# Kernel optimization log

Hardware: AMD Instinct MI355X
Metric: run time of the kernel (lower is better)

## Reference

```python
import jax, jax.numpy as jnp
import numpy as np

N_ATOMS = 50_000
N_EDGES = 1_600_000
N_ANGLES = 1_500_000
N_SPECIES = 16
DIM = 64
HID = [64, 64, 64]
IN_DIM = 1 + 2 * N_SPECIES  # theta + two onehot species encodings


def setup_inputs() -> dict:
    key = jax.random.key(0)
    ks = jax.random.split(key, 16)
    species = jax.random.randint(ks[0], (N_ATOMS,), 0, N_SPECIES)
    edge_dst = jax.random.randint(ks[1], (N_EDGES,), 0, N_ATOMS)
    # distances strictly positive (avoid blowup in 1/d)
    distances = jax.random.uniform(ks[2], (N_EDGES,), jnp.float32, 0.5, 1.5)
    switch = jax.random.uniform(ks[3], (N_EDGES,), jnp.float32)
    vec = jax.random.normal(ks[4], (N_EDGES, 3), jnp.float32)
    angle_src = jax.random.randint(ks[5], (N_ANGLES,), 0, N_EDGES)
    angle_dst = jax.random.randint(ks[6], (N_ANGLES,), 0, N_EDGES)
    central_atom = jax.random.randint(ks[7], (N_ANGLES,), 0, N_ATOMS)
    # FullyConnectedNet([64,64,64,64]) params, shared across the two calls
    dims = [IN_DIM] + HID + [DIM]
    params = {}
    for i in range(len(dims) - 1):
        fan_in = dims[i]
        params[f"W{i}"] = jax.random.normal(ks[8 + i], (dims[i], dims[i + 1]), jnp.float32) / np.sqrt(fan_in)
        params[f"b{i}"] = jnp.zeros((dims[i + 1],), jnp.float32)
    return dict(species=species, edge_dst=edge_dst, distances=distances,
                switch=switch, vec=vec, angle_src=angle_src, angle_dst=angle_dst,
                central_atom=central_atom, **params)


def _mlp(x, W0, b0, W1, b1, W2, b2, W3, b3):
    h = jax.nn.silu(x @ W0 + b0)
    h = jax.nn.silu(h @ W1 + b1)
    h = jax.nn.silu(h @ W2 + b2)
    return h @ W3 + b3  # linear output layer


def reference(species, edge_dst, distances, switch, vec, angle_src, angle_dst,
              central_atom, W0, b0, W1, b1, W2, b2, W3, b3):
    onehot = jax.nn.one_hot(species, N_SPECIES, dtype=jnp.float32)  # [N, 16]
    d = distances[:, None]
    sw = switch[:, None]
    vecn = vec / d
    sij = sw / d  # divide_distances=True
    Rij = jnp.concatenate((sij, sij * vecn), axis=-1)  # [E, 4]
    zdest = onehot[edge_dst]  # [E, 16]
    z_angsrc = zdest[angle_src]  # [A, 16]
    z_angdst = zdest[angle_dst]  # [A, 16]
    theta = jnp.sum(Rij[angle_src] * Rij[angle_dst], axis=-1, keepdims=True)  # [A, 1]
    Gijk = (_mlp(jnp.concatenate((theta, z_angsrc, z_angdst), axis=-1), W0, b0, W1, b1, W2, b2, W3, b3)
            + _mlp(jnp.concatenate((theta, z_angdst, z_angsrc), axis=-1), W0, b0, W1, b1, W2, b2, W3, b3))
    embedding = jax.ops.segment_sum(Gijk * theta, central_atom, species.shape[0])  # [N, 64]
    return embedding
```

## Files before the change

kernel.cpp:

```cpp
#include <hip/hip_runtime.h>

#define N_ATOMS   50000
#define N_EDGES   1600000
#define N_ANGLES  1500000
#define SCAN_B    196

#define NT      256
#define UMAX    4.852092f
#define H_U     0.038055623f
#define INV_HU  26.277306f
#define TSZ     (136 * NT * 64)

#define E_BLK   6250
#define P_BLK   112
#define Z_BLK   196

#define B_BLK   272
#define A_BLK   5860
#define R_BLK   8704
#define M_BLK   5860

typedef unsigned short u16;
typedef unsigned int   u32;
typedef _Float16 f16x8 __attribute__((ext_vector_type(8)));
typedef float    f32x4 __attribute__((ext_vector_type(4)));
typedef u16      u16x8 __attribute__((ext_vector_type(8)));

__device__ __forceinline__ float silu_f(float x) {
    return __fdividef(x, 1.0f + __expf(-x));
}
__device__ __forceinline__ u16 f2h(float x) {
    _Float16 h = (_Float16)x;
    return __builtin_bit_cast(u16, h);
}
__device__ __forceinline__ float h2f(u16 u) {
    return (float)__builtin_bit_cast(_Float16, u);
}

__global__ __launch_bounds__(256) void fused_prep_kernel(
    const float* __restrict__ distances, const float* __restrict__ sw,
    const float* __restrict__ vec, const int* __restrict__ edge_dst,
    const int* __restrict__ species,
    const float* __restrict__ W0, const float* __restrict__ b0,
    const float* __restrict__ W1, const float* __restrict__ W2,
    const float* __restrict__ W3,
    float2* __restrict__ EC8,
    u16* __restrict__ WT1, u16* __restrict__ WT2, u16* __restrict__ WT3,
    float* __restrict__ base_tab, int* __restrict__ cnt)
{
    const int bid = (int)blockIdx.x;
    const int tid = (int)threadIdx.x;

    if (bid < E_BLK) {
        int e = bid * 256 + tid;
        if (e >= N_EDGES) return;
        const float d   = distances[e];
        const float s   = sw[e];
        const float inv = 1.0f / d;
        const float sij = s * inv;
        const float c   = sij * inv;
        const int   sp  = species[edge_dst[e]];
        u16 h0 = f2h(sij);
        u16 h1 = f2h(c * vec[3*e+0]);
        u16 h2 = f2h(c * vec[3*e+1]);
        u16 h3 = f2h(c * vec[3*e+2]);
        h0 = (h0 & 0xFFFEu) | ((u16)( sp       & 1));
        h1 = (h1 & 0xFFFEu) | ((u16)((sp >> 1) & 1));
        h2 = (h2 & 0xFFFEu) | ((u16)((sp >> 2) & 1));
        h3 = (h3 & 0xFFFEu) | ((u16)((sp >> 3) & 1));
        const u32 lo = (u32)h0 | ((u32)h1 << 16);
        const u32 hi = (u32)h2 | ((u32)h3 << 16);
        EC8[e] = make_float2(__uint_as_float(lo), __uint_as_float(hi));
    } else if (bid < E_BLK + P_BLK) {
        int t = (bid - E_BLK) * 256 + tid;
        if (t < 3 * 4096) {
            int l = t >> 12, e = t & 4095, n = e >> 6, k = e & 63;
            const float* W = (l == 0) ? W1 : (l == 1) ? W2 : W3;
            u16* WT        = (l == 0) ? WT1 : (l == 1) ? WT2 : WT3;
            WT[n*64 + k] = f2h(W[k*64 + n]);
        }
        int u = t - 3 * 4096;
        if (u >= 0 && u < 256 * 64) {
            int sd = u >> 6, j = u & 63, s = sd >> 4, d = sd & 15;
            base_tab[u] = W0[(1+s)*64 + j] + W0[(17+d)*64 + j] + b0[j];
        }
    } else {
        int idx = (bid - E_BLK - P_BLK) * 256 + tid;
        if (idx < N_ATOMS) cnt[idx] = 0;
    }
}

__device__ __forceinline__ u32 make_rec(float2 Es, float2 Ed) {
    const u32 slo = __float_as_uint(Es.x), shi = __float_as_uint(Es.y);
    const u32 dlo = __float_as_uint(Ed.x), dhi = __float_as_uint(Ed.y);
    const int s1 = (int)((slo & 1u) | ((slo >> 15) & 2u)
                       | ((shi & 1u) << 2) | ((shi >> 13) & 8u));
    const int s2 = (int)((dlo & 1u) | ((dlo >> 15) & 2u)
                       | ((dhi & 1u) << 2) | ((dhi >> 13) & 8u));
    const float theta = h2f((u16)slo) * h2f((u16)dlo)
                      + h2f((u16)(slo >> 16)) * h2f((u16)(dlo >> 16))
                      + h2f((u16)shi) * h2f((u16)dhi)
                      + h2f((u16)(shi >> 16)) * h2f((u16)(dhi >> 16));
    const int s = min(s1, s2), d = max(s1, s2);
    const int pid = s*16 - (s*(s-1))/2 + (d - s);

    const float x  = theta * 0.125f;
    const float ax = fabsf(x);
    float uu = __logf(ax + __fsqrt_rn(fmaf(ax, ax, 1.0f)));
    uu = copysignf(uu, x);
    const float tt = fminf(fmaxf(fmaf(uu, INV_HU, UMAX * INV_HU), 0.0f),
                           (float)NT - 1.001f);
    const u32 tfx = (u32)(tt * 32768.0f);
    return (tfx << 8) | (u32)pid;
}

__device__ __forceinline__ void dense_mfma(const u16* __restrict__ strip,
    const u16* __restrict__ WT, int r15, int g4, f32x4 acc[4][4])
{
    #pragma unroll
    for (int kt = 0; kt < 2; ++kt) {
        f16x8 A[4], B[4];
        #pragma unroll
        for (int mt = 0; mt < 4; ++mt) {
            int row = mt*16 + r15;
            int col = (kt*32 + g4*8) ^ ((row & 7) << 3);
            A[mt] = *(const f16x8*)&strip[row*64 + col];
        }
        #pragma unroll
        for (int nt = 0; nt < 4; ++nt)
            B[nt] = *(const f16x8*)&WT[(nt*16 + r15)*64 + kt*32 + g4*8];
        #pragma unroll
        for (int mt = 0; mt < 4; ++mt) {
            #pragma unroll
            for (int nt = 0; nt < 4; ++nt)
                acc[mt][nt] = __builtin_amdgcn_mfma_f32_16x16x32_f16(
                    A[mt], B[nt], acc[mt][nt], 0, 0, 0);
        }
    }
}

__device__ __forceinline__ void act_store(u16* __restrict__ strip,
    const float* __restrict__ bias, int r15, int g4, f32x4 acc[4][4])
{
    float bn[4];
    #pragma unroll
    for (int nt = 0; nt < 4; ++nt) bn[nt] = bias[nt*16 + r15];
    #pragma unroll
    for (int mt = 0; mt < 4; ++mt) {
        #pragma unroll
        for (int r = 0; r < 4; ++r) {
            int row = mt*16 + g4*4 + r;
            int rsw = (row & 7) << 3;
            #pragma unroll
            for (int nt = 0; nt < 4; ++nt)
                strip[row*64 + ((nt*16 + r15) ^ rsw)] =
                    f2h(silu_f(acc[mt][nt][r] + bn[nt]));
        }
    }
}

__global__ __launch_bounds__(256) void angle_build_kernel(
    const int* __restrict__ a_src, const int* __restrict__ a_dst,
    const int* __restrict__ a_ca, const float2* __restrict__ EC8,
    int* __restrict__ cnt, u32* __restrict__ car, u32* __restrict__ recU,
    const float* __restrict__ W0, const float* __restrict__ base_tab,
    const u16* __restrict__ WT1, const u16* __restrict__ WT2,
    const u16* __restrict__ WT3,
    const float* __restrict__ b1, const float* __restrict__ b2,
    const float* __restrict__ b3,
    u16* __restrict__ Tp)
{
    __shared__ __align__(16) u16 act[256 * 64];
    const int bid = (int)blockIdx.x;
    const int tid = (int)threadIdx.x;

    if (bid >= B_BLK) {
        int i = (bid - B_BLK) * 256 + tid;
        if (i >= N_ANGLES) return;
        const int se = a_src[i], de = a_dst[i], ca = a_ca[i];
        const float2 Es = EC8[se], Ed = EC8[de];
        const u32 rank = (u32)atomicAdd(&cnt[ca], 1);
        car[i]  = (rank << 18) | (u32)ca;
        recU[i] = make_rec(Es, Ed);
        return;
    }

    const int lane = tid & 63;
    const int wv   = tid >> 6;
    const int r15  = lane & 15;
    const int g4   = lane >> 4;

    const int pid = bid >> 1;
    const int m   = bid & 1;
    int s = 0, rem = pid;
    while (rem >= 16 - s) { rem -= 16 - s; ++s; }
    const int d = s + rem;

    const int idx = tid;
    const float u  = fmaf((float)idx, H_U, -UMAX);
    const float eu = __expf(u);
    const float theta = 4.0f * (eu - __frcp_rn(eu));

    u16* strip = act + wv * 4096;

    f32x4 accG[4][4];
    #pragma unroll
    for (int nt = 0; nt < 4; ++nt) {
        float bv = b3[nt*16 + r15];
        #pragma unroll
        for (int mt = 0; mt < 4; ++mt) accG[mt][nt] = {bv, bv, bv, bv};
    }

    {
        const int p = m ? (d*16 + s) : (s*16 + d);
        const float4* bs4 = (const float4*)(base_tab + p*64);
        const float4* w04 = (const float4*)W0;
        const int rsw = (lane & 7) << 3;
        #pragma unroll
        for (int c = 0; c < 8; ++c) {
            float4 bl = bs4[2*c], bh = bs4[2*c+1];
            float4 wl = w04[2*c], wh = w04[2*c+1];
            u16x8 hv;
            hv[0] = f2h(silu_f(fmaf(theta, wl.x, bl.x)));
            hv[1] = f2h(silu_f(fmaf(theta, wl.y, bl.y)));
            hv[2] = f2h(silu_f(fmaf(theta, wl.z, bl.z)));
            hv[3] = f2h(silu_f(fmaf(theta, wl.w, bl.w)));
            hv[4] = f2h(silu_f(fmaf(theta, wh.x, bh.x)));
            hv[5] = f2h(silu_f(fmaf(theta, wh.y, bh.y)));
            hv[6] = f2h(silu_f(fmaf(theta, wh.z, bh.z)));
            hv[7] = f2h(silu_f(fmaf(theta, wh.w, bh.w)));
            *(u16x8*)&strip[lane*64 + ((c*8) ^ rsw)] = hv;
        }
    }
    {
        f32x4 acc[4][4];
        #pragma unroll
        for (int mt = 0; mt < 4; ++mt)
            #pragma unroll
            for (int nt = 0; nt < 4; ++nt) acc[mt][nt] = {0.f,0.f,0.f,0.f};
        dense_mfma(strip, WT1, r15, g4, acc);
        act_store(strip, b1, r15, g4, acc);
    }
    {
        f32x4 acc[4][4];
        #pragma unroll
        for (int mt = 0; mt < 4; ++mt)
            #pragma unroll
            for (int nt = 0; nt < 4; ++nt) acc[mt][nt] = {0.f,0.f,0.f,0.f};
        dense_mfma(strip, WT2, r15, g4, acc);
        act_store(strip, b2, r15, g4, acc);
    }
    dense_mfma(strip, WT3, r15, g4, accG);

    #pragma unroll
    for (int mt = 0; mt < 4; ++mt) {
        #pragma unroll
        for (int r = 0; r < 4; ++r) {
            int row = mt*16 + g4*4 + r;
            int rsw = (row & 7) << 3;
            #pragma unroll
            for (int nt = 0; nt < 4; ++nt)
                strip[row*64 + ((nt*16 + r15) ^ rsw)] = f2h(accG[mt][nt][r]);
        }
    }
    __syncthreads();

    u16* dst = Tp + (size_t)m * TSZ + ((size_t)pid * NT + (size_t)idx) * 64;
    const int rsw = (tid & 7) << 3;
    #pragma unroll
    for (int c = 0; c < 8; ++c)
        *(u16x8*)(dst + c*8) = *(const u16x8*)&act[tid*64 + ((c*8) ^ rsw)];
}

__global__ __launch_bounds__(1024) void scanAB_kernel(
    const int* __restrict__ cnt, int* __restrict__ boff)
{
    __shared__ int sh[1024];
    const int t = (int)threadIdx.x;
    const int base = t * 64;
    int v = 0;
    #pragma unroll 8
    for (int k = 0; k < 64; ++k) {
        int idx = base + k;
        if (idx < N_ATOMS) v += cnt[idx];
    }
    sh[t] = v;
    __syncthreads();
    for (int off = 1; off < 1024; off <<= 1) {
        int u = (t >= off) ? sh[t - off] : 0;
        __syncthreads();
        sh[t] += u;
        __syncthreads();
    }
    if ((t & 3) == 0 && (t >> 2) < SCAN_B) boff[t >> 2] = sh[t] - v;
}

__global__ __launch_bounds__(256) void scanC_kernel(
    const int* __restrict__ cnt, const int* __restrict__ boff,
    int* __restrict__ cursor)
{
    __shared__ int sh[256];
    const int t = (int)threadIdx.x;
    const int idx = (int)blockIdx.x * 256 + t;
    int v = (idx < N_ATOMS) ? cnt[idx] : 0;
    sh[t] = v;
    __syncthreads();
    for (int off = 1; off < 256; off <<= 1) {
        int u = (t >= off) ? sh[t - off] : 0;
        __syncthreads();
        sh[t] += u;
        __syncthreads();
    }
    if (idx < N_ATOMS) {
        cursor[idx] = boff[blockIdx.x] + sh[t] - v;
        if (idx == N_ATOMS - 1) cursor[N_ATOMS] = boff[blockIdx.x] + sh[t];
    }
}

__global__ __launch_bounds__(256) void permute_repack_kernel(
    const u32* __restrict__ recU, const u32* __restrict__ car,
    const int* __restrict__ cursor, u32* __restrict__ rec,
    const u16* __restrict__ Tp, u32* __restrict__ T2)
{
    const int bid = (int)blockIdx.x;
    const int tid = (int)threadIdx.x;

    if (bid < R_BLK) {
        int idx = bid * 256 + tid;
        if (idx >= TSZ) return;
        const int row = (idx >> 6) & (NT - 1);
        const int nxt = (row < NT - 1) ? idx + 64 : idx;
        const int rown = (row < NT - 1) ? row + 1 : row;
        const float ua  = fmaf((float)row,  H_U, -UMAX);
        const float ub  = fmaf((float)rown, H_U, -UMAX);
        const float ea  = __expf(ua), eb = __expf(ub);
        const float tha = 4.0f * (ea - __frcp_rn(ea));
        const float thb = 4.0f * (eb - __frcp_rn(eb));
        const float ha = (h2f(Tp[idx]) + h2f(Tp[TSZ + idx])) * tha;
        const float hb = (h2f(Tp[nxt]) + h2f(Tp[TSZ + nxt])) * thb;
        T2[idx] = (u32)f2h(ha) | ((u32)f2h(hb) << 16);
    } else {
        int i = (bid - R_BLK) * 256 + tid;
        if (i >= N_ANGLES) return;
        const u32 cr = car[i];
        const int ca   = (int)(cr & 0x3FFFFu);
        const int rank = (int)(cr >> 18);
        rec[cursor[ca] + rank] = recU[i];
    }
}

__global__ __launch_bounds__(256) void lookup_kernel(
    const u32* __restrict__ rec, const int* __restrict__ cursor,
    const u32* __restrict__ T2, float* __restrict__ out)
{
    const int tid  = (int)threadIdx.x;
    const int lane = tid & 63;
    const int wv   = tid >> 6;
    const int atom = (int)blockIdx.x * 4 + wv;
    if (atom >= N_ATOMS) return;

    const int start = cursor[atom];
    const int end   = cursor[atom + 1];

    float acc0 = 0.f, acc1 = 0.f, acc2 = 0.f, acc3 = 0.f;
    for (int base = start; base < end; base += 64) {
        const int len = min(64, end - base);
        const int wp  = (int)rec[base + min(lane, len - 1)];

        int j = 0;
        for (; j + 3 < len; j += 4) {
            const u32 w0 = (u32)__shfl(wp, j),     w1 = (u32)__shfl(wp, j + 1);
            const u32 w2 = (u32)__shfl(wp, j + 2), w3 = (u32)__shfl(wp, j + 3);
            const u32 pr0 = T2[((w0 & 255u) << 14) + ((w0 >> 23) << 6) + (u32)lane];
            const u32 pr1 = T2[((w1 & 255u) << 14) + ((w1 >> 23) << 6) + (u32)lane];
            const u32 pr2 = T2[((w2 & 255u) << 14) + ((w2 >> 23) << 6) + (u32)lane];
            const u32 pr3 = T2[((w3 & 255u) << 14) + ((w3 >> 23) << 6) + (u32)lane];
            const float fr0 = (float)((w0 >> 8) & 32767u) * (1.0f / 32768.0f);
            const float fr1 = (float)((w1 >> 8) & 32767u) * (1.0f / 32768.0f);
            const float fr2 = (float)((w2 >> 8) & 32767u) * (1.0f / 32768.0f);
            const float fr3 = (float)((w3 >> 8) & 32767u) * (1.0f / 32768.0f);
            float ga, gb;
            ga = h2f((u16)(pr0 & 0xFFFFu)); gb = h2f((u16)(pr0 >> 16));
            acc0 += fmaf(fr0, gb - ga, ga);
            ga = h2f((u16)(pr1 & 0xFFFFu)); gb = h2f((u16)(pr1 >> 16));
            acc1 += fmaf(fr1, gb - ga, ga);
            ga = h2f((u16)(pr2 & 0xFFFFu)); gb = h2f((u16)(pr2 >> 16));
            acc2 += fmaf(fr2, gb - ga, ga);
            ga = h2f((u16)(pr3 & 0xFFFFu)); gb = h2f((u16)(pr3 >> 16));
            acc3 += fmaf(fr3, gb - ga, ga);
        }
        for (; j < len; ++j) {
            const u32 w  = (u32)__shfl(wp, j);
            const u32 pr = T2[((w & 255u) << 14) + ((w >> 23) << 6) + (u32)lane];
            const float fr = (float)((w >> 8) & 32767u) * (1.0f / 32768.0f);
            const float ga = h2f((u16)(pr & 0xFFFFu));
            const float gb = h2f((u16)(pr >> 16));
            acc0 += fmaf(fr, gb - ga, ga);
        }
    }
    out[(size_t)atom * 64 + lane] = (acc0 + acc1) + (acc2 + acc3);
}

extern "C" void kernel_launch(void* const* d_in, const int* in_sizes, int n_in,
                              void* d_out, int out_size, void* d_ws, size_t ws_size,
                              hipStream_t stream) {
    const int*   species   = (const int*)  d_in[0];
    const int*   edge_dst  = (const int*)  d_in[1];
    const float* distances = (const float*)d_in[2];
    const float* sw        = (const float*)d_in[3];
    const float* vec       = (const float*)d_in[4];
    const int*   a_src     = (const int*)  d_in[5];
    const int*   a_dst     = (const int*)  d_in[6];
    const int*   a_ca      = (const int*)  d_in[7];
    const float* W0 = (const float*)d_in[8];
    const float* b0 = (const float*)d_in[9];
    const float* W1 = (const float*)d_in[10];
    const float* b1 = (const float*)d_in[11];
    const float* W2 = (const float*)d_in[12];
    const float* b2 = (const float*)d_in[13];
    const float* W3 = (const float*)d_in[14];
    const float* b3 = (const float*)d_in[15];
    float* out = (float*)d_out;

    float2* EC8    = (float2*)d_ws;
    int*    cnt    = (int*)(EC8 + N_EDGES);
    int*    cursor = cnt + N_ATOMS;
    int*    boff   = cursor + N_ATOMS + 1;
    u32*    car    = (u32*)(boff + SCAN_B + 3);
    u32*    recU   = car + N_ANGLES;
    u32*    rec    = recU + N_ANGLES;
    u16*    WT1    = (u16*)(rec + N_ANGLES);
    u16*    WT2    = WT1 + 4096;
    u16*    WT3    = WT2 + 4096;
    float*  base_tab = (float*)(WT3 + 4096);
    u16*    Tp     = (u16*)(base_tab + 256*64);
    u32*    T2     = (u32*)(Tp + 2 * TSZ);

    fused_prep_kernel<<<E_BLK + P_BLK + Z_BLK, 256, 0, stream>>>(
        distances, sw, vec, edge_dst, species,
        W0, b0, W1, W2, W3, EC8, WT1, WT2, WT3, base_tab, cnt);
    angle_build_kernel<<<B_BLK + A_BLK, 256, 0, stream>>>(
        a_src, a_dst, a_ca, EC8, cnt, car, recU,
        W0, base_tab, WT1, WT2, WT3, b1, b2, b3, Tp);
    scanAB_kernel<<<1, 1024, 0, stream>>>(cnt, boff);
    scanC_kernel<<<SCAN_B, 256, 0, stream>>>(cnt, boff, cursor);
    permute_repack_kernel<<<R_BLK + M_BLK, 256, 0, stream>>>(
        recU, car, cursor, rec, Tp, T2);
    lookup_kernel<<<(N_ATOMS + 3) / 4, 256, 0, stream>>>(rec, cursor, T2, out);
}
```

Measured before the change: 199.3 us.

## Move MLP table build into edge-prep kernel and stage weights in LDS

The MLP lookup-table build blocks move out of the angle kernel and into the first kernel, next to the edge-encoding and counter-zeroing blocks. The weight transpose and base-table precompute are removed: each table block now stages W1/W2/W3 into swizzled LDS itself and sums the W0 rows inline. The angle record/atomic work becomes its own kernel. The aim is to drop a prep dependency and let the table MFMA work overlap with the bandwidth-bound edge pass. The cost is extra barriers, 8KB more LDS per block, and redundant fp32-to-fp16 weight conversion in every table block.

After: 209.9 us. 5.3% more time.

```diff
diff --git a/kernel.cpp b/kernel.cpp
--- a/kernel.cpp
+++ b/kernel.cpp
@@ -11,12 +11,10 @@
 #define INV_HU  26.277306f
 #define TSZ     (136 * NT * 64)
 
+#define B_BLK   272
 #define E_BLK   6250
-#define P_BLK   112
 #define Z_BLK   196
 
-#define B_BLK   272
-#define A_BLK   5860
 #define R_BLK   8704
 #define M_BLK   5860
 
@@ -35,59 +33,6 @@
 }
 __device__ __forceinline__ float h2f(u16 u) {
     return (float)__builtin_bit_cast(_Float16, u);
-}
-
-__global__ __launch_bounds__(256) void fused_prep_kernel(
-    const float* __restrict__ distances, const float* __restrict__ sw,
-    const float* __restrict__ vec, const int* __restrict__ edge_dst,
-    const int* __restrict__ species,
-    const float* __restrict__ W0, const float* __restrict__ b0,
-    const float* __restrict__ W1, const float* __restrict__ W2,
-    const float* __restrict__ W3,
-    float2* __restrict__ EC8,
-    u16* __restrict__ WT1, u16* __restrict__ WT2, u16* __restrict__ WT3,
-    float* __restrict__ base_tab, int* __restrict__ cnt)
-{
-    const int bid = (int)blockIdx.x;
-    const int tid = (int)threadIdx.x;
-
-    if (bid < E_BLK) {
-        int e = bid * 256 + tid;
-        if (e >= N_EDGES) return;
-        const float d   = distances[e];
-        const float s   = sw[e];
-        const float inv = 1.0f / d;
-        const float sij = s * inv;
-        const float c   = sij * inv;
-        const int   sp  = species[edge_dst[e]];
-        u16 h0 = f2h(sij);
-        u16 h1 = f2h(c * vec[3*e+0]);
-        u16 h2 = f2h(c * vec[3*e+1]);
-        u16 h3 = f2h(c * vec[3*e+2]);
-        h0 = (h0 & 0xFFFEu) | ((u16)( sp       & 1));
-        h1 = (h1 & 0xFFFEu) | ((u16)((sp >> 1) & 1));
-        h2 = (h2 & 0xFFFEu) | ((u16)((sp >> 2) & 1));
-        h3 = (h3 & 0xFFFEu) | ((u16)((sp >> 3) & 1));
-        const u32 lo = (u32)h0 | ((u32)h1 << 16);
-        const u32 hi = (u32)h2 | ((u32)h3 << 16);
-        EC8[e] = make_float2(__uint_as_float(lo), __uint_as_float(hi));
-    } else if (bid < E_BLK + P_BLK) {
-        int t = (bid - E_BLK) * 256 + tid;
-        if (t < 3 * 4096) {
-            int l = t >> 12, e = t & 4095, n = e >> 6, k = e & 63;
-            const float* W = (l == 0) ? W1 : (l == 1) ? W2 : W3;
-            u16* WT        = (l == 0) ? WT1 : (l == 1) ? WT2 : WT3;
-            WT[n*64 + k] = f2h(W[k*64 + n]);
-        }
-        int u = t - 3 * 4096;
-        if (u >= 0 && u < 256 * 64) {
-            int sd = u >> 6, j = u & 63, s = sd >> 4, d = sd & 15;
-            base_tab[u] = W0[(1+s)*64 + j] + W0[(17+d)*64 + j] + b0[j];
-        }
-    } else {
-        int idx = (bid - E_BLK - P_BLK) * 256 + tid;
-        if (idx < N_ATOMS) cnt[idx] = 0;
-    }
 }
 
 __device__ __forceinline__ u32 make_rec(float2 Es, float2 Ed) {
@@ -114,8 +59,19 @@
     return (tfx << 8) | (u32)pid;
 }
 
-__device__ __forceinline__ void dense_mfma(const u16* __restrict__ strip,
-    const u16* __restrict__ WT, int r15, int g4, f32x4 acc[4][4])
+__device__ __forceinline__ void stage_wt(const float* __restrict__ W,
+                                         u16* __restrict__ wt, int tid)
+{
+    #pragma unroll
+    for (int q = 0; q < 16; ++q) {
+        const int idx = q * 256 + tid;
+        const int k = idx >> 6, n = idx & 63;
+        wt[n*64 + ((((k >> 3) ^ (n & 7))) << 3) + (k & 7)] = f2h(W[idx]);
+    }
+}
+
+__device__ __forceinline__ void dense_mfma_lds(const u16* __restrict__ strip,
+    const u16* __restrict__ wt, int r15, int g4, f32x4 acc[4][4])
 {
     #pragma unroll
     for (int kt = 0; kt < 2; ++kt) {
@@ -126,9 +82,12 @@
             int col = (kt*32 + g4*8) ^ ((row & 7) << 3);
             A[mt] = *(const f16x8*)&strip[row*64 + col];
         }
-        #pragma unroll
-        for (int nt = 0; nt < 4; ++nt)
-            B[nt] = *(const f16x8*)&WT[(nt*16 + r15)*64 + kt*32 + g4*8];
+        const int k8 = kt*4 + g4;
+        #pragma unroll
+        for (int nt = 0; nt < 4; ++nt) {
+            const int n = nt*16 + r15;
+            B[nt] = *(const f16x8*)&wt[n*64 + ((k8 ^ (n & 7)) << 3)];
+        }
         #pragma unroll
         for (int mt = 0; mt < 4; ++mt) {
             #pragma unroll
@@ -159,29 +118,47 @@
     }
 }
 
-__global__ __launch_bounds__(256) void angle_build_kernel(
-    const int* __restrict__ a_src, const int* __restrict__ a_dst,
-    const int* __restrict__ a_ca, const float2* __restrict__ EC8,
-    int* __restrict__ cnt, u32* __restrict__ car, u32* __restrict__ recU,
-    const float* __restrict__ W0, const float* __restrict__ base_tab,
-    const u16* __restrict__ WT1, const u16* __restrict__ WT2,
-    const u16* __restrict__ WT3,
+__global__ __launch_bounds__(256) void prep_build_kernel(
+    const float* __restrict__ distances, const float* __restrict__ sw,
+    const float* __restrict__ vec, const int* __restrict__ edge_dst,
+    const int* __restrict__ species,
+    const float* __restrict__ W0, const float* __restrict__ b0,
+    const float* __restrict__ W1, const float* __restrict__ W2,
+    const float* __restrict__ W3,
     const float* __restrict__ b1, const float* __restrict__ b2,
     const float* __restrict__ b3,
-    u16* __restrict__ Tp)
+    float2* __restrict__ EC8, int* __restrict__ cnt, u16* __restrict__ Tp)
 {
     __shared__ __align__(16) u16 act[256 * 64];
+    __shared__ __align__(16) u16 wt[64 * 64];
     const int bid = (int)blockIdx.x;
     const int tid = (int)threadIdx.x;
 
     if (bid >= B_BLK) {
-        int i = (bid - B_BLK) * 256 + tid;
-        if (i >= N_ANGLES) return;
-        const int se = a_src[i], de = a_dst[i], ca = a_ca[i];
-        const float2 Es = EC8[se], Ed = EC8[de];
-        const u32 rank = (u32)atomicAdd(&cnt[ca], 1);
-        car[i]  = (rank << 18) | (u32)ca;
-        recU[i] = make_rec(Es, Ed);
+        if (bid < B_BLK + E_BLK) {
+            int e = (bid - B_BLK) * 256 + tid;
+            if (e >= N_EDGES) return;
+            const float d   = distances[e];
+            const float s   = sw[e];
+            const float inv = 1.0f / d;
+            const float sij = s * inv;
+            const float c   = sij * inv;
+            const int   sp  = species[edge_dst[e]];
+            u16 h0 = f2h(sij);
+            u16 h1 = f2h(c * vec[3*e+0]);
+            u16 h2 = f2h(c * vec[3*e+1]);
+            u16 h3 = f2h(c * vec[3*e+2]);
+            h0 = (h0 & 0xFFFEu) | ((u16)( sp       & 1));
+            h1 = (h1 & 0xFFFEu) | ((u16)((sp >> 1) & 1));
+            h2 = (h2 & 0xFFFEu) | ((u16)((sp >> 2) & 1));
+            h3 = (h3 & 0xFFFEu) | ((u16)((sp >> 3) & 1));
+            const u32 lo = (u32)h0 | ((u32)h1 << 16);
+            const u32 hi = (u32)h2 | ((u32)h3 << 16);
+            EC8[e] = make_float2(__uint_as_float(lo), __uint_as_float(hi));
+        } else {
+            int idx = (bid - B_BLK - E_BLK) * 256 + tid;
+            if (idx < N_ATOMS) cnt[idx] = 0;
+        }
         return;
     }
 
@@ -212,14 +189,23 @@
     }
 
     {
-        const int p = m ? (d*16 + s) : (s*16 + d);
-        const float4* bs4 = (const float4*)(base_tab + p*64);
+        const int rA = m ? d : s;
+        const int rB = m ? s : d;
         const float4* w04 = (const float4*)W0;
+        const float4* wA  = (const float4*)(W0 + (1  + rA) * 64);
+        const float4* wB  = (const float4*)(W0 + (17 + rB) * 64);
+        const float4* b04 = (const float4*)b0;
         const int rsw = (lane & 7) << 3;
         #pragma unroll
         for (int c = 0; c < 8; ++c) {
-            float4 bl = bs4[2*c], bh = bs4[2*c+1];
-            float4 wl = w04[2*c], wh = w04[2*c+1];
+            float4 a1 = wA[2*c],   a2 = wA[2*c+1];
+            float4 v1 = wB[2*c],   v2 = wB[2*c+1];
+            float4 c1 = b04[2*c],  c2 = b04[2*c+1];
+            float4 wl = w04[2*c],  wh = w04[2*c+1];
+            float4 bl = make_float4(a1.x+v1.x+c1.x, a1.y+v1.y+c1.y,
+                                    a1.z+v1.z+c1.z, a1.w+v1.w+c1.w);
+            float4 bh = make_float4(a2.x+v2.x+c2.x, a2.y+v2.y+c2.y,
+                                    a2.z+v2.z+c2.z, a2.w+v2.w+c2.w);
             u16x8 hv;
             hv[0] = f2h(silu_f(fmaf(theta, wl.x, bl.x)));
             hv[1] = f2h(silu_f(fmaf(theta, wl.y, bl.y)));
@@ -232,25 +218,33 @@
             *(u16x8*)&strip[lane*64 + ((c*8) ^ rsw)] = hv;
         }
     }
+    stage_wt(W1, wt, tid);
+    __syncthreads();
     {
         f32x4 acc[4][4];
         #pragma unroll
         for (int mt = 0; mt < 4; ++mt)
             #pragma unroll
             for (int nt = 0; nt < 4; ++nt) acc[mt][nt] = {0.f,0.f,0.f,0.f};
-        dense_mfma(strip, WT1, r15, g4, acc);
+        dense_mfma_lds(strip, wt, r15, g4, acc);
         act_store(strip, b1, r15, g4, acc);
     }
+    __syncthreads();
+    stage_wt(W2, wt, tid);
+    __syncthreads();
     {
         f32x4 acc[4][4];
         #pragma unroll
         for (int mt = 0; mt < 4; ++mt)
             #pragma unroll
             for (int nt = 0; nt < 4; ++nt) acc[mt][nt] = {0.f,0.f,0.f,0.f};
-        dense_mfma(strip, WT2, r15, g4, acc);
+        dense_mfma_lds(strip, wt, r15, g4, acc);
         act_store(strip, b2, r15, g4, acc);
     }
-    dense_mfma(strip, WT3, r15, g4, accG);
+    __syncthreads();
+    stage_wt(W3, wt, tid);
+    __syncthreads();
+    dense_mfma_lds(strip, wt, r15, g4, accG);
 
     #pragma unroll
     for (int mt = 0; mt < 4; ++mt) {
@@ -270,6 +264,20 @@
     #pragma unroll
     for (int c = 0; c < 8; ++c)
         *(u16x8*)(dst + c*8) = *(const u16x8*)&act[tid*64 + ((c*8) ^ rsw)];
+}
+
+__global__ __launch_bounds__(256) void angle_prep_kernel(
+    const int* __restrict__ a_src, const int* __restrict__ a_dst,
+    const int* __restrict__ a_ca, const float2* __restrict__ EC8,
+    int* __restrict__ cnt, u32* __restrict__ car, u32* __restrict__ recU)
+{
+    int i = (int)blockIdx.x * 256 + (int)threadIdx.x;
+    if (i >= N_ANGLES) return;
+    const int se = a_src[i], de = a_dst[i], ca = a_ca[i];
+    const float2 Es = EC8[se], Ed = EC8[de];
+    const u32 rank = (u32)atomicAdd(&cnt[ca], 1);
+    car[i]  = (rank << 18) | (u32)ca;
+    recU[i] = make_rec(Es, Ed);
 }
 
 __global__ __launch_bounds__(1024) void scanAB_kernel(
@@ -429,19 +437,14 @@
     u32*    car    = (u32*)(boff + SCAN_B + 3);
     u32*    recU   = car + N_ANGLES;
     u32*    rec    = recU + N_ANGLES;
-    u16*    WT1    = (u16*)(rec + N_ANGLES);
-    u16*    WT2    = WT1 + 4096;
-    u16*    WT3    = WT2 + 4096;
-    float*  base_tab = (float*)(WT3 + 4096);
-    u16*    Tp     = (u16*)(base_tab + 256*64);
+    u16*    Tp     = (u16*)(rec + N_ANGLES);
     u32*    T2     = (u32*)(Tp + 2 * TSZ);
 
-    fused_prep_kernel<<<E_BLK + P_BLK + Z_BLK, 256, 0, stream>>>(
+    prep_build_kernel<<<B_BLK + E_BLK + Z_BLK, 256, 0, stream>>>(
         distances, sw, vec, edge_dst, species,
-        W0, b0, W1, W2, W3, EC8, WT1, WT2, WT3, base_tab, cnt);
-    angle_build_kernel<<<B_BLK + A_BLK, 256, 0, stream>>>(
-        a_src, a_dst, a_ca, EC8, cnt, car, recU,
-        W0, base_tab, WT1, WT2, WT3, b1, b2, b3, Tp);
+        W0, b0, W1, W2, W3, b1, b2, b3, EC8, cnt, Tp);
+    angle_prep_kernel<<<(N_ANGLES + 255) / 256, 256, 0, stream>>>(
+        a_src, a_dst, a_ca, EC8, cnt, car, recU);
     scanAB_kernel<<<1, 1024, 0, stream>>>(cnt, boff);
     scanC_kernel<<<SCAN_B, 256, 0, stream>>>(cnt, boff, cursor);
     permute_repack_kernel<<<R_BLK + M_BLK, 256, 0, stream>>>(
```
